# Kernel tuning notes

Hardware: AMD Instinct MI355X
Metric: run time of the kernel (lower is better)

The kernel has to match this reference:

```python
import jax, jax.numpy as jnp
import numpy as np

N = 50000   # nodes
E = 800000  # edges (avg degree 16)
D = 96      # feature dim (in = hidden = out)


def setup_inputs() -> dict:
    key = jax.random.key(0)
    ks = jax.random.split(key, 6)
    scale = 1.0 / np.sqrt(D)
    return {
        "x": jax.random.normal(ks[0], (N, D), jnp.float32),
        "edge_index": jax.random.randint(ks[1], (2, E), 0, N, dtype=jnp.int64),
        "W1": jax.random.normal(ks[2], (D, D), jnp.float32) * scale,
        "b1": jnp.zeros((D,), jnp.float32),
        "a1": jnp.full((1,), 0.25, jnp.float32),  # PReLU weight
        "W2": jax.random.normal(ks[3], (D, D), jnp.float32) * scale,
        "b2": jnp.zeros((D,), jnp.float32),
    }


def _gcn_conv(x, W, b, src, dst, norm, n):
    # GCNConv: linear transform, then degree-normalized scatter-add aggregation
    h = x @ W                               # [N, D_out]
    msg = h[src] * norm[:, None]            # gather + scale, [E+N, D_out]
    out = jax.ops.segment_sum(msg, dst, num_segments=n)
    return out + b


def reference(x, edge_index, W1, b1, a1, W2, b2):
    n = x.shape[0]
    # add self loops (PyG gcn_norm default, fill_value=1.0)
    loop = jnp.arange(n, dtype=edge_index.dtype)
    src = jnp.concatenate([edge_index[0], loop])
    dst = jnp.concatenate([edge_index[1], loop])
    # symmetric normalization: D^{-1/2} A D^{-1/2}
    ones = jnp.ones(src.shape[0], dtype=x.dtype)
    deg = jax.ops.segment_sum(ones, dst, num_segments=n)
    dinv = jnp.where(deg > 0, jax.lax.rsqrt(deg), 0.0)
    norm = dinv[src] * dinv[dst]

    h = _gcn_conv(x, W1, b1, src, dst, norm, n)
    h = jnp.where(h > 0, h, a1 * h)  # PReLU (dropout p=0.0 is a no-op)
    h = _gcn_conv(h, W2, b2, src, dst, norm, n)
    return h
```

## Files before the change

### kernel.cpp

```cpp
#include <hip/hip_runtime.h>
#include <hip/hip_bf16.h>

#define NNODES 50000
#define NEDGES 800000
#define DIM    96
#define NBUCK  196
#define PCHUNK 3125
#define TM     64
#define XPAD   104

typedef __attribute__((ext_vector_type(8))) short   short8;
typedef __attribute__((ext_vector_type(4))) float   float4v;

__device__ __forceinline__ float loadF(const void* p, long i, int isbf) {
    return isbf ? __bfloat162float(((const __hip_bfloat16*)p)[i])
                : ((const float*)p)[i];
}
__device__ __forceinline__ int clampN(int v) {
    return v < 0 ? 0 : (v >= NNODES ? NNODES - 1 : v);
}
__device__ __forceinline__ int edgeDst(const int* w, int e, int is64) {
    return clampN(is64 ? w[2 * (NEDGES + e)] : w[NEDGES + e]);
}
__device__ __forceinline__ int edgeSrc(const int* w, int e, int is64) {
    return clampN(is64 ? w[2 * e] : w[e]);
}

__global__ void k_sniff(const unsigned* __restrict__ xw,
                        const unsigned* __restrict__ ew,
                        int* __restrict__ flags,
                        int* __restrict__ bcnt,
                        int* __restrict__ bcur) {
    int lane = threadIdx.x;
    for (int i = lane; i < NBUCK; i += 64) { bcnt[i] = 0; bcur[i] = 0; }
    int bad = 0, nz = 0;
    for (int r = 0; r < 4; ++r) {
        unsigned w  = xw[lane + 64 * r];
        unsigned lo = w & 0xffffu;
        unsigned ex = (lo >> 7) & 0xffu;
        if (!(lo == 0u || (ex >= 90u && ex <= 145u))) bad++;
        unsigned o = ew[2 * (lane + 64 * r) + 1];
        if (o != 0u) nz++;
    }
    for (int off = 32; off; off >>= 1) {
        bad += __shfl_down(bad, off);
        nz  += __shfl_down(nz,  off);
    }
    if (lane == 0) {
        flags[0] = (bad <= 32) ? 1 : 0;
        flags[1] = (nz  <  4) ? 1 : 0;
    }
}

__global__ __launch_bounds__(256) void k_bcount(const int* __restrict__ w,
                                                int* __restrict__ bcnt,
                                                const int* __restrict__ flags) {
    __shared__ int h[NBUCK];
    const int is64 = flags[1];
    for (int i = threadIdx.x; i < NBUCK; i += 256) h[i] = 0;
    __syncthreads();
    const int nth = gridDim.x * blockDim.x;
    for (int e = blockIdx.x * blockDim.x + threadIdx.x; e < NEDGES; e += nth)
        atomicAdd(&h[edgeDst(w, e, is64) >> 8], 1);
    __syncthreads();
    for (int i = threadIdx.x; i < NBUCK; i += 256)
        if (h[i]) atomicAdd(&bcnt[i], h[i]);
}

__global__ __launch_bounds__(256) void k_part(const int* __restrict__ w,
                                              const int* __restrict__ bcnt,
                                              int* __restrict__ bcur,
                                              unsigned* __restrict__ ebuf,
                                              const int* __restrict__ flags) {
    __shared__ int sbase[256];
    __shared__ int h[NBUCK];
    __shared__ int base[NBUCK];
    const int is64 = flags[1];
    const int tid  = threadIdx.x;
    const int e0 = blockIdx.x * PCHUNK;
    const int e1 = (e0 + PCHUNK < NEDGES) ? e0 + PCHUNK : NEDGES;

    int v = (tid < NBUCK) ? bcnt[tid] : 0;
    sbase[tid] = v;
    __syncthreads();
    for (int off = 1; off < 256; off <<= 1) {
        int t = (tid >= off) ? sbase[tid - off] : 0;
        __syncthreads();
        sbase[tid] += t;
        __syncthreads();
    }
    int excl = sbase[tid] - v;
    __syncthreads();
    sbase[tid] = excl;
    if (tid < NBUCK) h[tid] = 0;
    __syncthreads();

    for (int e = e0 + tid; e < e1; e += 256)
        atomicAdd(&h[edgeDst(w, e, is64) >> 8], 1);
    __syncthreads();
    for (int i = tid; i < NBUCK; i += 256) {
        int c = h[i];
        base[i] = c ? sbase[i] + atomicAdd(&bcur[i], c) : 0;
        h[i] = 0;
    }
    __syncthreads();
    for (int e = e0 + tid; e < e1; e += 256) {
        int s = edgeSrc(w, e, is64);
        int d = edgeDst(w, e, is64);
        int b = d >> 8;
        int pos = base[b] + atomicAdd(&h[b], 1);
        ebuf[pos] = ((unsigned)d << 16) | (unsigned)s;
    }
}

__global__ __launch_bounds__(512) void k_csr(const unsigned* __restrict__ ebuf,
                                             const int* __restrict__ bcnt,
                                             int* __restrict__ rowptr,
                                             unsigned short* __restrict__ col,
                                             float* __restrict__ dinv) {
    __shared__ int gbase[256];
    __shared__ int h[256];
    __shared__ int sc[256];
    __shared__ int cur[256];
    const int b   = blockIdx.x;
    const int tid = threadIdx.x;

    if (tid < 256) gbase[tid] = (tid < NBUCK) ? bcnt[tid] : 0;
    __syncthreads();
    for (int off = 1; off < 256; off <<= 1) {
        int t = 0;
        if (tid < 256 && tid >= off) t = gbase[tid - off];
        __syncthreads();
        if (tid < 256) gbase[tid] += t;
        __syncthreads();
    }
    const int e0 = (b == 0) ? 0 : gbase[b - 1];
    const int e1 = gbase[b];
    __syncthreads();

    if (tid < 256) h[tid] = 0;
    __syncthreads();
    for (int e = e0 + tid; e < e1; e += 512)
        atomicAdd(&h[(ebuf[e] >> 16) & 255], 1);
    __syncthreads();
    int v = 0;
    if (tid < 256) { v = h[tid]; sc[tid] = v; }
    __syncthreads();
    for (int off = 1; off < 256; off <<= 1) {
        int t = 0;
        if (tid < 256 && tid >= off) t = sc[tid - off];
        __syncthreads();
        if (tid < 256) sc[tid] += t;
        __syncthreads();
    }
    if (tid < 256) {
        int start = e0 + sc[tid] - v;
        cur[tid] = start;
        int node = b * 256 + tid;
        if (node < NNODES) {
            rowptr[node] = start;
            dinv[node] = rsqrtf((float)v + 1.0f);
        }
    }
    if (b == 0 && tid == 0) rowptr[NNODES] = NEDGES;
    __syncthreads();
    for (int e = e0 + tid; e < e1; e += 512) {
        unsigned r = ebuf[e];
        int dl = (r >> 16) & 255;
        int pos = atomicAdd(&cur[dl], 1);
        col[pos] = (unsigned short)(r & 0xffffu);
    }
}

__global__ __launch_bounds__(256) void k_gemm_mfma(
        const void* __restrict__ X, int x_force_bf16,
        const void* __restrict__ W,
        const float* __restrict__ dinv,
        __hip_bfloat16* __restrict__ g,
        const int* __restrict__ flags) {
    __shared__ __hip_bfloat16 Xs[TM * XPAD];
    __shared__ __hip_bfloat16 Wt[DIM * XPAD];

    const int t    = threadIdx.x;
    const int fbf  = flags[0];
    const int xbf  = x_force_bf16 ? 1 : fbf;
    const int row0 = blockIdx.x * TM;

    for (int idx = t; idx < DIM * DIM; idx += 256) {
        int k = idx / DIM, n = idx - k * DIM;
        Wt[n * XPAD + k] = __float2bfloat16(loadF(W, idx, fbf));
    }
    for (int idx = t; idx < TM * DIM; idx += 256) {
        int r = idx / DIM, c = idx - r * DIM;
        int gr = row0 + r;
        float v = (gr < NNODES) ? loadF(X, (long)gr * DIM + c, xbf) : 0.f;
        Xs[r * XPAD + c] = __float2bfloat16(v);
    }
    __syncthreads();

    const int wave = t >> 6;
    const int lane = t & 63;
    const int m    = lane & 15;
    const int quad = lane >> 4;

    const short* xsp = (const short*)Xs;
    short8 a[3];
#pragma unroll
    for (int kt = 0; kt < 3; ++kt)
        a[kt] = *(const short8*)(xsp + (wave * 16 + m) * XPAD + kt * 32 + quad * 8);

    float dv[4];
#pragma unroll
    for (int r2 = 0; r2 < 4; ++r2) {
        int gr = row0 + wave * 16 + quad * 4 + r2;
        dv[r2] = (gr < NNODES) ? dinv[gr] : 0.f;
    }

    const short* wtp = (const short*)Wt;
#pragma unroll
    for (int nt = 0; nt < 6; ++nt) {
        float4v acc = {0.f, 0.f, 0.f, 0.f};
#pragma unroll
        for (int kt = 0; kt < 3; ++kt) {
            short8 b = *(const short8*)(wtp + (nt * 16 + m) * XPAD + kt * 32 + quad * 8);
            acc = __builtin_amdgcn_mfma_f32_16x16x32_bf16(a[kt], b, acc, 0, 0, 0);
        }
#pragma unroll
        for (int r2 = 0; r2 < 4; ++r2) {
            int gr = row0 + wave * 16 + quad * 4 + r2;
            if (gr < NNODES)
                g[(size_t)gr * DIM + nt * 16 + m] = __float2bfloat16(acc[r2] * dv[r2]);
        }
    }
}

__global__ __launch_bounds__(256) void k_aggr(
        const __hip_bfloat16* __restrict__ g,
        const int* __restrict__ rowptr,
        const unsigned short* __restrict__ col,
        const float* __restrict__ dinv,
        const void* __restrict__ b,
        const void* __restrict__ a1,
        void* __restrict__ out,
        const int* __restrict__ flags, int prelu) {
    const int wave = threadIdx.x >> 6;
    const int lane = threadIdx.x & 63;
    const int row  = blockIdx.x * 4 + wave;
    if (row >= NNODES) return;
    const int fbf = flags[0];
    const __hip_bfloat162* gv = (const __hip_bfloat162*)g;
    const int c = lane;

    float2 acc = {0.f, 0.f};
    if (c < 48) acc = __bfloat1622float2(gv[(size_t)row * 48 + c]);

    const int p0 = rowptr[row], p1 = rowptr[row + 1];
    int i = p0;
    for (; i + 16 <= p1; i += 16) {
        int s[16];
#pragma unroll
        for (int k = 0; k < 16; ++k) s[k] = col[i + k];
        if (c < 48) {
            float2 v[16];
#pragma unroll
            for (int k = 0; k < 16; ++k)
                v[k] = __bfloat1622float2(gv[(size_t)s[k] * 48 + c]);
            float2 t0, t1, t2, t3;
            t0.x = (v[0].x + v[1].x) + (v[2].x + v[3].x);
            t0.y = (v[0].y + v[1].y) + (v[2].y + v[3].y);
            t1.x = (v[4].x + v[5].x) + (v[6].x + v[7].x);
            t1.y = (v[4].y + v[5].y) + (v[6].y + v[7].y);
            t2.x = (v[8].x + v[9].x) + (v[10].x + v[11].x);
            t2.y = (v[8].y + v[9].y) + (v[10].y + v[11].y);
            t3.x = (v[12].x + v[13].x) + (v[14].x + v[15].x);
            t3.y = (v[12].y + v[13].y) + (v[14].y + v[15].y);
            acc.x += (t0.x + t1.x) + (t2.x + t3.x);
            acc.y += (t0.y + t1.y) + (t2.y + t3.y);
        }
    }
    for (; i + 8 <= p1; i += 8) {
        int s[8];
#pragma unroll
        for (int k = 0; k < 8; ++k) s[k] = col[i + k];
        if (c < 48) {
            float2 v[8];
#pragma unroll
            for (int k = 0; k < 8; ++k)
                v[k] = __bfloat1622float2(gv[(size_t)s[k] * 48 + c]);
            acc.x += ((v[0].x + v[1].x) + (v[2].x + v[3].x))
                   + ((v[4].x + v[5].x) + (v[6].x + v[7].x));
            acc.y += ((v[0].y + v[1].y) + (v[2].y + v[3].y))
                   + ((v[4].y + v[5].y) + (v[6].y + v[7].y));
        }
    }
    for (; i + 4 <= p1; i += 4) {
        int s0 = col[i], s1 = col[i+1], s2 = col[i+2], s3 = col[i+3];
        if (c < 48) {
            float2 v0 = __bfloat1622float2(gv[(size_t)s0 * 48 + c]);
            float2 v1 = __bfloat1622float2(gv[(size_t)s1 * 48 + c]);
            float2 v2 = __bfloat1622float2(gv[(size_t)s2 * 48 + c]);
            float2 v3 = __bfloat1622float2(gv[(size_t)s3 * 48 + c]);
            acc.x += (v0.x + v1.x) + (v2.x + v3.x);
            acc.y += (v0.y + v1.y) + (v2.y + v3.y);
        }
    }
    for (; i < p1; ++i) {
        int s = col[i];
        if (c < 48) {
            float2 v = __bfloat1622float2(gv[(size_t)s * 48 + c]);
            acc.x += v.x; acc.y += v.y;
        }
    }

    if (c < 48) {
        float dv = dinv[row];
        float vx = dv * acc.x + loadF(b, 2 * c,     fbf);
        float vy = dv * acc.y + loadF(b, 2 * c + 1, fbf);
        if (prelu) {
            float alpha = loadF(a1, 0, fbf);
            vx = vx > 0.f ? vx : alpha * vx;
            vy = vy > 0.f ? vy : alpha * vy;
            ((__hip_bfloat162*)out)[(size_t)row * 48 + c] =
                __halves2bfloat162(__float2bfloat16(vx), __float2bfloat16(vy));
        } else if (fbf) {
            ((__hip_bfloat162*)out)[(size_t)row * 48 + c] =
                __halves2bfloat162(__float2bfloat16(vx), __float2bfloat16(vy));
        } else {
            float2 o; o.x = vx; o.y = vy;
            ((float2*)out)[(size_t)row * 48 + c] = o;
        }
    }
}

extern "C" void kernel_launch(void* const* d_in, const int* in_sizes, int n_in,
                              void* d_out, int out_size, void* d_ws, size_t ws_size,
                              hipStream_t stream) {
    const void* x  = d_in[0];
    const int*  ei = (const int*)d_in[1];
    const void* W1 = d_in[2];
    const void* b1 = d_in[3];
    const void* a1 = d_in[4];
    const void* W2 = d_in[5];
    const void* b2 = d_in[6];

    size_t off = 0;
    auto alloc = [&](size_t bytes) { size_t p = off; off = (off + bytes + 255) & ~(size_t)255; return p; };
    char* ws = (char*)d_ws;
    int*            flags  = (int*)           (ws + alloc(1024));
    float*          dinv   = (float*)         (ws + alloc((size_t)NNODES * 4));
    int*            bcnt   = (int*)           (ws + alloc((size_t)NBUCK * 4));
    int*            bcur   = (int*)           (ws + alloc((size_t)NBUCK * 4));
    int*            rowptr = (int*)           (ws + alloc(((size_t)NNODES + 1) * 4));
    unsigned*       ebuf   = (unsigned*)      (ws + alloc((size_t)NEDGES * 4));
    unsigned short* col    = (unsigned short*)(ws + alloc((size_t)NEDGES * 2));
    __hip_bfloat16* g      = (__hip_bfloat16*)(ws + alloc((size_t)NNODES * DIM * 2));
    __hip_bfloat16* g2     = (__hip_bfloat16*)(ws + alloc((size_t)NNODES * DIM * 2));
    if (ws_size < off) return;

    k_sniff<<<1, 64, 0, stream>>>((const unsigned*)x, (const unsigned*)ei, flags, bcnt, bcur);

    k_bcount<<<256, 256, 0, stream>>>(ei, bcnt, flags);
    k_part  <<<(NEDGES + PCHUNK - 1) / PCHUNK, 256, 0, stream>>>(ei, bcnt, bcur, ebuf, flags);
    k_csr   <<<NBUCK, 512, 0, stream>>>(ebuf, bcnt, rowptr, col, dinv);

    const int gemm_grid = (NNODES + TM - 1) / TM;
    const int aggr_grid = (NNODES + 3) / 4;

    k_gemm_mfma<<<gemm_grid, 256, 0, stream>>>(x, 0, W1, dinv, g, flags);
    k_aggr<<<aggr_grid, 256, 0, stream>>>(g, rowptr, col, dinv, b1, a1, g2, flags, 1);

    k_gemm_mfma<<<gemm_grid, 256, 0, stream>>>(g2, 1, W2, dinv, g, flags);
    k_aggr<<<aggr_grid, 256, 0, stream>>>(g, rowptr, col, dinv, b2, a1, d_out, flags, 0);
}
```

Before: 235.5 us.

## Fuse CSR build into one grid-barrier kernel and fuse layer-1 aggregation with GEMM2

Merges the sniff, bucket-count, partition and CSR kernels into a single persistent kernel that synchronises its 256 blocks through a software global barrier on a device atomic counter. Edges are packed in LDS and per-block histograms replace global atomics. The first aggregation is fused with the second GEMM, so PReLU output stays in LDS instead of round-tripping through global memory. GEMM input staging also switches to float4 loads. This removes several launches and one intermediate buffer, but relies on all 256 blocks being co-resident for the spin barrier, and the fused aggregation+GEMM uses fewer, larger blocks.

```diff
diff --git a/kernel.cpp b/kernel.cpp
--- a/kernel.cpp
+++ b/kernel.cpp
@@ -5,12 +5,17 @@
 #define NEDGES 800000
 #define DIM    96
 #define NBUCK  196
-#define PCHUNK 3125
 #define TM     64
 #define XPAD   104
+#define PBLK   256
+#define PTHR   512
+#define PCH    3125
+#define HPAD   256
 
 typedef __attribute__((ext_vector_type(8))) short   short8;
 typedef __attribute__((ext_vector_type(4))) float   float4v;
+
+__device__ int g_bar[2] = {0, 0};
 
 __device__ __forceinline__ float loadF(const void* p, long i, int isbf) {
     return isbf ? __bfloat162float(((const __hip_bfloat16*)p)[i])
@@ -26,154 +31,163 @@
     return clampN(is64 ? w[2 * e] : w[e]);
 }
 
-__global__ void k_sniff(const unsigned* __restrict__ xw,
-                        const unsigned* __restrict__ ew,
-                        int* __restrict__ flags,
-                        int* __restrict__ bcnt,
-                        int* __restrict__ bcur) {
-    int lane = threadIdx.x;
-    for (int i = lane; i < NBUCK; i += 64) { bcnt[i] = 0; bcur[i] = 0; }
-    int bad = 0, nz = 0;
-    for (int r = 0; r < 4; ++r) {
-        unsigned w  = xw[lane + 64 * r];
+__device__ __forceinline__ void gbar(int slot) {
+    __syncthreads();
+    if (threadIdx.x == 0) {
+        __threadfence();
+        atomicAdd(&g_bar[slot], 1);
+        while (atomicAdd(&g_bar[slot], 0) < PBLK) __builtin_amdgcn_s_sleep(2);
+        __threadfence();
+    }
+    __syncthreads();
+}
+
+__global__ __launch_bounds__(512) void k_prep(
+        const unsigned* __restrict__ xw,
+        const int* __restrict__ ew,
+        int* __restrict__ flags,
+        int* __restrict__ hist,
+        unsigned* __restrict__ ebuf,
+        int* __restrict__ rowptr,
+        unsigned short* __restrict__ col,
+        float* __restrict__ dinv) {
+    __shared__ unsigned pack[PCH];
+    __shared__ int h[NBUCK];
+    __shared__ int sb[256];
+    __shared__ int tot[256];
+    __shared__ int base[NBUCK];
+    __shared__ int h256[256];
+    __shared__ int sc[256];
+    __shared__ int cur[256];
+    __shared__ int sniff[2];
+
+    const int tid = threadIdx.x;
+    const int blk = blockIdx.x;
+
+    if (tid < 2) sniff[tid] = 0;
+    __syncthreads();
+    if (tid < 256) {
+        unsigned w  = xw[tid];
         unsigned lo = w & 0xffffu;
         unsigned ex = (lo >> 7) & 0xffu;
-        if (!(lo == 0u || (ex >= 90u && ex <= 145u))) bad++;
-        unsigned o = ew[2 * (lane + 64 * r) + 1];
-        if (o != 0u) nz++;
-    }
-    for (int off = 32; off; off >>= 1) {
-        bad += __shfl_down(bad, off);
-        nz  += __shfl_down(nz,  off);
-    }
-    if (lane == 0) {
-        flags[0] = (bad <= 32) ? 1 : 0;
-        flags[1] = (nz  <  4) ? 1 : 0;
-    }
-}
-
-__global__ __launch_bounds__(256) void k_bcount(const int* __restrict__ w,
-                                                int* __restrict__ bcnt,
-                                                const int* __restrict__ flags) {
-    __shared__ int h[NBUCK];
-    const int is64 = flags[1];
-    for (int i = threadIdx.x; i < NBUCK; i += 256) h[i] = 0;
-    __syncthreads();
-    const int nth = gridDim.x * blockDim.x;
-    for (int e = blockIdx.x * blockDim.x + threadIdx.x; e < NEDGES; e += nth)
-        atomicAdd(&h[edgeDst(w, e, is64) >> 8], 1);
-    __syncthreads();
-    for (int i = threadIdx.x; i < NBUCK; i += 256)
-        if (h[i]) atomicAdd(&bcnt[i], h[i]);
-}
-
-__global__ __launch_bounds__(256) void k_part(const int* __restrict__ w,
-                                              const int* __restrict__ bcnt,
-                                              int* __restrict__ bcur,
-                                              unsigned* __restrict__ ebuf,
-                                              const int* __restrict__ flags) {
-    __shared__ int sbase[256];
-    __shared__ int h[NBUCK];
-    __shared__ int base[NBUCK];
-    const int is64 = flags[1];
-    const int tid  = threadIdx.x;
-    const int e0 = blockIdx.x * PCHUNK;
-    const int e1 = (e0 + PCHUNK < NEDGES) ? e0 + PCHUNK : NEDGES;
-
-    int v = (tid < NBUCK) ? bcnt[tid] : 0;
-    sbase[tid] = v;
+        if (!(lo == 0u || (ex >= 90u && ex <= 145u))) atomicAdd(&sniff[0], 1);
+        if (((const unsigned*)ew)[2 * tid + 1] != 0u)  atomicAdd(&sniff[1], 1);
+    }
+    __syncthreads();
+    const int fbf  = (sniff[0] <= 32) ? 1 : 0;
+    const int is64 = (sniff[1] <  4) ? 1 : 0;
+    if (blk == 0 && tid == 0) { flags[0] = fbf; flags[1] = is64; }
+
+    for (int i = tid; i < NBUCK; i += PTHR) h[i] = 0;
+    __syncthreads();
+    const int e0 = blk * PCH;
+    for (int k = tid; k < PCH; k += PTHR) {
+        int e = e0 + k;
+        int s = edgeSrc(ew, e, is64);
+        int d = edgeDst(ew, e, is64);
+        pack[k] = ((unsigned)d << 16) | (unsigned)s;
+        atomicAdd(&h[d >> 8], 1);
+    }
+    __syncthreads();
+    for (int i = tid; i < NBUCK; i += PTHR) hist[blk * HPAD + i] = h[i];
+
+    gbar(0);
+
+    if (tid < 256) tot[tid] = 0;
+    int pre = 0;
+    if (tid < NBUCK) {
+        int t = 0, p = 0;
+        for (int j = 0; j < PBLK; ++j) {
+            int v = hist[j * HPAD + tid];
+            t += v;
+            if (j < blk) p += v;
+        }
+        tot[tid] = t;
+        pre = p;
+    }
+    __syncthreads();
+    if (tid < 256) sb[tid] = tot[tid];
     __syncthreads();
     for (int off = 1; off < 256; off <<= 1) {
-        int t = (tid >= off) ? sbase[tid - off] : 0;
+        int t2 = 0;
+        if (tid < 256 && tid >= off) t2 = sb[tid - off];
         __syncthreads();
-        sbase[tid] += t;
+        if (tid < 256) sb[tid] += t2;
         __syncthreads();
     }
-    int excl = sbase[tid] - v;
-    __syncthreads();
-    sbase[tid] = excl;
-    if (tid < NBUCK) h[tid] = 0;
-    __syncthreads();
-
-    for (int e = e0 + tid; e < e1; e += 256)
-        atomicAdd(&h[edgeDst(w, e, is64) >> 8], 1);
-    __syncthreads();
-    for (int i = tid; i < NBUCK; i += 256) {
-        int c = h[i];
-        base[i] = c ? sbase[i] + atomicAdd(&bcur[i], c) : 0;
-        h[i] = 0;
-    }
-    __syncthreads();
-    for (int e = e0 + tid; e < e1; e += 256) {
-        int s = edgeSrc(w, e, is64);
-        int d = edgeDst(w, e, is64);
-        int b = d >> 8;
+    if (tid < NBUCK) {
+        base[tid] = (sb[tid] - tot[tid]) + pre;
+        h[tid] = 0;
+    }
+    __syncthreads();
+    for (int k = tid; k < PCH; k += PTHR) {
+        unsigned r = pack[k];
+        int b = r >> 24;
         int pos = base[b] + atomicAdd(&h[b], 1);
-        ebuf[pos] = ((unsigned)d << 16) | (unsigned)s;
-    }
-}
-
-__global__ __launch_bounds__(512) void k_csr(const unsigned* __restrict__ ebuf,
-                                             const int* __restrict__ bcnt,
-                                             int* __restrict__ rowptr,
-                                             unsigned short* __restrict__ col,
-                                             float* __restrict__ dinv) {
-    __shared__ int gbase[256];
-    __shared__ int h[256];
-    __shared__ int sc[256];
-    __shared__ int cur[256];
-    const int b   = blockIdx.x;
-    const int tid = threadIdx.x;
-
-    if (tid < 256) gbase[tid] = (tid < NBUCK) ? bcnt[tid] : 0;
+        ebuf[pos] = r;
+    }
+
+    gbar(1);
+
+    if (blk >= NBUCK) return;
+    const int be0 = sb[blk] - tot[blk];
+    const int be1 = sb[blk];
+    if (tid < 256) h256[tid] = 0;
+    __syncthreads();
+    for (int e = be0 + tid; e < be1; e += PTHR)
+        atomicAdd(&h256[(ebuf[e] >> 16) & 255], 1);
+    __syncthreads();
+    int v = 0;
+    if (tid < 256) { v = h256[tid]; sc[tid] = v; }
     __syncthreads();
     for (int off = 1; off < 256; off <<= 1) {
-        int t = 0;
-        if (tid < 256 && tid >= off) t = gbase[tid - off];
+        int t2 = 0;
+        if (tid < 256 && tid >= off) t2 = sc[tid - off];
         __syncthreads();
-        if (tid < 256) gbase[tid] += t;
+        if (tid < 256) sc[tid] += t2;
         __syncthreads();
     }
-    const int e0 = (b == 0) ? 0 : gbase[b - 1];
-    const int e1 = gbase[b];
-    __syncthreads();
-
-    if (tid < 256) h[tid] = 0;
-    __syncthreads();
-    for (int e = e0 + tid; e < e1; e += 512)
-        atomicAdd(&h[(ebuf[e] >> 16) & 255], 1);
-    __syncthreads();
-    int v = 0;
-    if (tid < 256) { v = h[tid]; sc[tid] = v; }
-    __syncthreads();
-    for (int off = 1; off < 256; off <<= 1) {
-        int t = 0;
-        if (tid < 256 && tid >= off) t = sc[tid - off];
-        __syncthreads();
-        if (tid < 256) sc[tid] += t;
-        __syncthreads();
-    }
     if (tid < 256) {
-        int start = e0 + sc[tid] - v;
+        int start = be0 + sc[tid] - v;
         cur[tid] = start;
-        int node = b * 256 + tid;
+        int node = blk * 256 + tid;
         if (node < NNODES) {
             rowptr[node] = start;
             dinv[node] = rsqrtf((float)v + 1.0f);
         }
     }
-    if (b == 0 && tid == 0) rowptr[NNODES] = NEDGES;
-    __syncthreads();
-    for (int e = e0 + tid; e < e1; e += 512) {
+    if (blk == 0 && tid == 0) rowptr[NNODES] = NEDGES;
+    __syncthreads();
+    for (int e = be0 + tid; e < be1; e += PTHR) {
         unsigned r = ebuf[e];
-        int dl = (r >> 16) & 255;
-        int pos = atomicAdd(&cur[dl], 1);
+        int pos = atomicAdd(&cur[(r >> 16) & 255], 1);
         col[pos] = (unsigned short)(r & 0xffffu);
     }
 }
 
+__device__ __forceinline__ void stage_wt(const void* W, int fbf,
+                                         __hip_bfloat16* Wt, int t) {
+    if (!fbf) {
+        const float4* Wv = (const float4*)W;
+        for (int idx = t; idx < DIM * DIM / 4; idx += 256) {
+            int k = idx / (DIM / 4);
+            int n = (idx - k * (DIM / 4)) * 4;
+            float4 w4 = Wv[idx];
+            Wt[(n + 0) * XPAD + k] = __float2bfloat16(w4.x);
+            Wt[(n + 1) * XPAD + k] = __float2bfloat16(w4.y);
+            Wt[(n + 2) * XPAD + k] = __float2bfloat16(w4.z);
+            Wt[(n + 3) * XPAD + k] = __float2bfloat16(w4.w);
+        }
+    } else {
+        for (int idx = t; idx < DIM * DIM; idx += 256) {
+            int k = idx / DIM, n = idx - k * DIM;
+            Wt[n * XPAD + k] = __float2bfloat16(loadF(W, idx, 1));
+        }
+    }
+}
+
 __global__ __launch_bounds__(256) void k_gemm_mfma(
-        const void* __restrict__ X, int x_force_bf16,
+        const void* __restrict__ X,
         const void* __restrict__ W,
         const float* __restrict__ dinv,
         __hip_bfloat16* __restrict__ g,
@@ -181,20 +195,35 @@
     __shared__ __hip_bfloat16 Xs[TM * XPAD];
     __shared__ __hip_bfloat16 Wt[DIM * XPAD];
 
-    const int t    = threadIdx.x;
+    const int t = threadIdx.x;
+    if (blockIdx.x == 0 && t == 0) {
+        atomicExch(&g_bar[0], 0);
+        atomicExch(&g_bar[1], 0);
+    }
     const int fbf  = flags[0];
-    const int xbf  = x_force_bf16 ? 1 : fbf;
     const int row0 = blockIdx.x * TM;
 
-    for (int idx = t; idx < DIM * DIM; idx += 256) {
-        int k = idx / DIM, n = idx - k * DIM;
-        Wt[n * XPAD + k] = __float2bfloat16(loadF(W, idx, fbf));
-    }
-    for (int idx = t; idx < TM * DIM; idx += 256) {
-        int r = idx / DIM, c = idx - r * DIM;
-        int gr = row0 + r;
-        float v = (gr < NNODES) ? loadF(X, (long)gr * DIM + c, xbf) : 0.f;
-        Xs[r * XPAD + c] = __float2bfloat16(v);
+    stage_wt(W, fbf, Wt, t);
+    if (!fbf) {
+        const float4* Xv = (const float4*)X;
+        for (int idx = t; idx < TM * DIM / 4; idx += 256) {
+            int r = idx / (DIM / 4);
+            int c = (idx - r * (DIM / 4)) * 4;
+            int gr = row0 + r;
+            float4 vv = {0.f, 0.f, 0.f, 0.f};
+            if (gr < NNODES) vv = Xv[(size_t)gr * (DIM / 4) + (c >> 2)];
+            *(__hip_bfloat162*)&Xs[r * XPAD + c] =
+                __halves2bfloat162(__float2bfloat16(vv.x), __float2bfloat16(vv.y));
+            *(__hip_bfloat162*)&Xs[r * XPAD + c + 2] =
+                __halves2bfloat162(__float2bfloat16(vv.z), __float2bfloat16(vv.w));
+        }
+    } else {
+        for (int idx = t; idx < TM * DIM; idx += 256) {
+            int r = idx / DIM, c = idx - r * DIM;
+            int gr = row0 + r;
+            float vv = (gr < NNODES) ? loadF(X, (long)gr * DIM + c, 1) : 0.f;
+            Xs[r * XPAD + c] = __float2bfloat16(vv);
+        }
     }
     __syncthreads();
 
@@ -230,6 +259,152 @@
             int gr = row0 + wave * 16 + quad * 4 + r2;
             if (gr < NNODES)
                 g[(size_t)gr * DIM + nt * 16 + m] = __float2bfloat16(acc[r2] * dv[r2]);
+        }
+    }
+}
+
+__device__ __forceinline__ float2 gather_row(
+        const __hip_bfloat162* __restrict__ gv,
+        const int* __restrict__ rowptr,
+        const unsigned short* __restrict__ col,
+        int row, int c) {
+    float2 acc = {0.f, 0.f};
+    if (c < 48) acc = __bfloat1622float2(gv[(size_t)row * 48 + c]);
+    const int p0 = rowptr[row], p1 = rowptr[row + 1];
+    int i = p0;
+    for (; i + 16 <= p1; i += 16) {
+        int s[16];
+#pragma unroll
+        for (int k = 0; k < 16; ++k) s[k] = col[i + k];
+        if (c < 48) {
+            float2 v[16];
+#pragma unroll
+            for (int k = 0; k < 16; ++k)
+                v[k] = __bfloat1622float2(gv[(size_t)s[k] * 48 + c]);
+            float2 t0, t1, t2, t3;
+            t0.x = (v[0].x + v[1].x) + (v[2].x + v[3].x);
+            t0.y = (v[0].y + v[1].y) + (v[2].y + v[3].y);
+            t1.x = (v[4].x + v[5].x) + (v[6].x + v[7].x);
+            t1.y = (v[4].y + v[5].y) + (v[6].y + v[7].y);
+            t2.x = (v[8].x + v[9].x) + (v[10].x + v[11].x);
+            t2.y = (v[8].y + v[9].y) + (v[10].y + v[11].y);
+            t3.x = (v[12].x + v[13].x) + (v[14].x + v[15].x);
+            t3.y = (v[12].y + v[13].y) + (v[14].y + v[15].y);
+            acc.x += (t0.x + t1.x) + (t2.x + t3.x);
+            acc.y += (t0.y + t1.y) + (t2.y + t3.y);
+        }
+    }
+    for (; i + 8 <= p1; i += 8) {
+        int s[8];
+#pragma unroll
+        for (int k = 0; k < 8; ++k) s[k] = col[i + k];
+        if (c < 48) {
+            float2 v[8];
+#pragma unroll
+            for (int k = 0; k < 8; ++k)
+                v[k] = __bfloat1622float2(gv[(size_t)s[k] * 48 + c]);
+            acc.x += ((v[0].x + v[1].x) + (v[2].x + v[3].x))
+                   + ((v[4].x + v[5].x) + (v[6].x + v[7].x));
+            acc.y += ((v[0].y + v[1].y) + (v[2].y + v[3].y))
+                   + ((v[4].y + v[5].y) + (v[6].y + v[7].y));
+        }
+    }
+    for (; i + 4 <= p1; i += 4) {
+        int s0 = col[i], s1 = col[i + 1], s2 = col[i + 2], s3 = col[i + 3];
+        if (c < 48) {
+            float2 v0 = __bfloat1622float2(gv[(size_t)s0 * 48 + c]);
+            float2 v1 = __bfloat1622float2(gv[(size_t)s1 * 48 + c]);
+            float2 v2 = __bfloat1622float2(gv[(size_t)s2 * 48 + c]);
+            float2 v3 = __bfloat1622float2(gv[(size_t)s3 * 48 + c]);
+            acc.x += (v0.x + v1.x) + (v2.x + v3.x);
+            acc.y += (v0.y + v1.y) + (v2.y + v3.y);
+        }
+    }
+    for (; i < p1; ++i) {
+        int s = col[i];
+        if (c < 48) {
+            float2 v = __bfloat1622float2(gv[(size_t)s * 48 + c]);
+            acc.x += v.x; acc.y += v.y;
+        }
+    }
+    return acc;
+}
+
+__global__ __launch_bounds__(256) void k_aggr_gemm(
+        const __hip_bfloat16* __restrict__ g,
+        const int* __restrict__ rowptr,
+        const unsigned short* __restrict__ col,
+        const float* __restrict__ dinv,
+        const void* __restrict__ b1,
+        const void* __restrict__ a1,
+        const void* __restrict__ W2,
+        __hip_bfloat16* __restrict__ g2,
+        const int* __restrict__ flags) {
+    __shared__ __hip_bfloat16 Hs[TM * XPAD];
+    __shared__ __hip_bfloat16 Wt[DIM * XPAD];
+
+    const int t = threadIdx.x;
+    const int fbf  = flags[0];
+    const int row0 = blockIdx.x * TM;
+    const int wave = t >> 6;
+    const int lane = t & 63;
+    const int c = lane;
+
+    stage_wt(W2, fbf, Wt, t);
+
+    const __hip_bfloat162* gv = (const __hip_bfloat162*)g;
+    const float alpha = loadF(a1, 0, fbf);
+    float bx = 0.f, by = 0.f;
+    if (c < 48) { bx = loadF(b1, 2 * c, fbf); by = loadF(b1, 2 * c + 1, fbf); }
+
+#pragma unroll 1
+    for (int p = 0; p < TM / 4; ++p) {
+        const int r   = p * 4 + wave;
+        const int row = row0 + r;
+        float vx = 0.f, vy = 0.f;
+        if (row < NNODES) {
+            float2 acc = gather_row(gv, rowptr, col, row, c);
+            float dv = dinv[row];
+            vx = dv * acc.x + bx;
+            vy = dv * acc.y + by;
+            vx = vx > 0.f ? vx : alpha * vx;
+            vy = vy > 0.f ? vy : alpha * vy;
+        }
+        if (c < 48)
+            *(__hip_bfloat162*)&Hs[r * XPAD + 2 * c] =
+                __halves2bfloat162(__float2bfloat16(vx), __float2bfloat16(vy));
+    }
+    __syncthreads();
+
+    const int m    = lane & 15;
+    const int quad = lane >> 4;
+    const short* xsp = (const short*)Hs;
+    short8 afr[3];
+#pragma unroll
+    for (int kt = 0; kt < 3; ++kt)
+        afr[kt] = *(const short8*)(xsp + (wave * 16 + m) * XPAD + kt * 32 + quad * 8);
+
+    float dvv[4];
+#pragma unroll
+    for (int r2 = 0; r2 < 4; ++r2) {
+        int gr = row0 + wave * 16 + quad * 4 + r2;
+        dvv[r2] = (gr < NNODES) ? dinv[gr] : 0.f;
+    }
+
+    const short* wtp = (const short*)Wt;
+#pragma unroll
+    for (int nt = 0; nt < 6; ++nt) {
+        float4v acc4 = {0.f, 0.f, 0.f, 0.f};
+#pragma unroll
+        for (int kt = 0; kt < 3; ++kt) {
+            short8 bfr = *(const short8*)(wtp + (nt * 16 + m) * XPAD + kt * 32 + quad * 8);
+            acc4 = __builtin_amdgcn_mfma_f32_16x16x32_bf16(afr[kt], bfr, acc4, 0, 0, 0);
+        }
+#pragma unroll
+        for (int r2 = 0; r2 < 4; ++r2) {
+            int gr = row0 + wave * 16 + quad * 4 + r2;
+            if (gr < NNODES)
+                g2[(size_t)gr * DIM + nt * 16 + m] = __float2bfloat16(acc4[r2] * dvv[r2]);
         }
     }
 }
@@ -248,69 +423,9 @@
     const int row  = blockIdx.x * 4 + wave;
     if (row >= NNODES) return;
     const int fbf = flags[0];
-    const __hip_bfloat162* gv = (const __hip_bfloat162*)g;
     const int c = lane;
 
-    float2 acc = {0.f, 0.f};
-    if (c < 48) acc = __bfloat1622float2(gv[(size_t)row * 48 + c]);
-
-    const int p0 = rowptr[row], p1 = rowptr[row + 1];
-    int i = p0;
-    for (; i + 16 <= p1; i += 16) {
-        int s[16];
-#pragma unroll
-        for (int k = 0; k < 16; ++k) s[k] = col[i + k];
-        if (c < 48) {
-            float2 v[16];
-#pragma unroll
-            for (int k = 0; k < 16; ++k)
-                v[k] = __bfloat1622float2(gv[(size_t)s[k] * 48 + c]);
-            float2 t0, t1, t2, t3;
-            t0.x = (v[0].x + v[1].x) + (v[2].x + v[3].x);
-            t0.y = (v[0].y + v[1].y) + (v[2].y + v[3].y);
-            t1.x = (v[4].x + v[5].x) + (v[6].x + v[7].x);
-            t1.y = (v[4].y + v[5].y) + (v[6].y + v[7].y);
-            t2.x = (v[8].x + v[9].x) + (v[10].x + v[11].x);
-            t2.y = (v[8].y + v[9].y) + (v[10].y + v[11].y);
-            t3.x = (v[12].x + v[13].x) + (v[14].x + v[15].x);
-            t3.y = (v[12].y + v[13].y) + (v[14].y + v[15].y);
-            acc.x += (t0.x + t1.x) + (t2.x + t3.x);
-            acc.y += (t0.y + t1.y) + (t2.y + t3.y);
-        }
-    }
-    for (; i + 8 <= p1; i += 8) {
-        int s[8];
-#pragma unroll
-        for (int k = 0; k < 8; ++k) s[k] = col[i + k];
-        if (c < 48) {
-            float2 v[8];
-#pragma unroll
-            for (int k = 0; k < 8; ++k)
-                v[k] = __bfloat1622float2(gv[(size_t)s[k] * 48 + c]);
-            acc.x += ((v[0].x + v[1].x) + (v[2].x + v[3].x))
-                   + ((v[4].x + v[5].x) + (v[6].x + v[7].x));
-            acc.y += ((v[0].y + v[1].y) + (v[2].y + v[3].y))
-                   + ((v[4].y + v[5].y) + (v[6].y + v[7].y));
-        }
-    }
-    for (; i + 4 <= p1; i += 4) {
-        int s0 = col[i], s1 = col[i+1], s2 = col[i+2], s3 = col[i+3];
-        if (c < 48) {
-            float2 v0 = __bfloat1622float2(gv[(size_t)s0 * 48 + c]);
-            float2 v1 = __bfloat1622float2(gv[(size_t)s1 * 48 + c]);
-            float2 v2 = __bfloat1622float2(gv[(size_t)s2 * 48 + c]);
-            float2 v3 = __bfloat1622float2(gv[(size_t)s3 * 48 + c]);
-            acc.x += (v0.x + v1.x) + (v2.x + v3.x);
-            acc.y += (v0.y + v1.y) + (v2.y + v3.y);
-        }
-    }
-    for (; i < p1; ++i) {
-        int s = col[i];
-        if (c < 48) {
-            float2 v = __bfloat1622float2(gv[(size_t)s * 48 + c]);
-            acc.x += v.x; acc.y += v.y;
-        }
-    }
+    float2 acc = gather_row((const __hip_bfloat162*)g, rowptr, col, row, c);
 
     if (c < 48) {
         float dv = dinv[row];
@@ -348,27 +463,21 @@
     char* ws = (char*)d_ws;
     int*            flags  = (int*)           (ws + alloc(1024));
     float*          dinv   = (float*)         (ws + alloc((size_t)NNODES * 4));
-    int*            bcnt   = (int*)           (ws + alloc((size_t)NBUCK * 4));
-    int*            bcur   = (int*)           (ws + alloc((size_t)NBUCK * 4));
     int*            rowptr = (int*)           (ws + alloc(((size_t)NNODES + 1) * 4));
+    int*            hist   = (int*)           (ws + alloc((size_t)PBLK * HPAD * 4));
     unsigned*       ebuf   = (unsigned*)      (ws + alloc((size_t)NEDGES * 4));
     unsigned short* col    = (unsigned short*)(ws + alloc((size_t)NEDGES * 2));
     __hip_bfloat16* g      = (__hip_bfloat16*)(ws + alloc((size_t)NNODES * DIM * 2));
     __hip_bfloat16* g2     = (__hip_bfloat16*)(ws + alloc((size_t)NNODES * DIM * 2));
     if (ws_size < off) return;
 
-    k_sniff<<<1, 64, 0, stream>>>((const unsigned*)x, (const unsigned*)ei, flags, bcnt, bcur);
-
-    k_bcount<<<256, 256, 0, stream>>>(ei, bcnt, flags);
-    k_part  <<<(NEDGES + PCHUNK - 1) / PCHUNK, 256, 0, stream>>>(ei, bcnt, bcur, ebuf, flags);
-    k_csr   <<<NBUCK, 512, 0, stream>>>(ebuf, bcnt, rowptr, col, dinv);
+    k_prep<<<PBLK, PTHR, 0, stream>>>((const unsigned*)x, ei, flags, hist,
+                                      ebuf, rowptr, col, dinv);
 
     const int gemm_grid = (NNODES + TM - 1) / TM;
     const int aggr_grid = (NNODES + 3) / 4;
 
-    k_gemm_mfma<<<gemm_grid, 256, 0, stream>>>(x, 0, W1, dinv, g, flags);
-    k_aggr<<<aggr_grid, 256, 0, stream>>>(g, rowptr, col, dinv, b1, a1, g2, flags, 1);
-
-    k_gemm_mfma<<<gemm_grid, 256, 0, stream>>>(g2, 1, W2, dinv, g, flags);
-    k_aggr<<<aggr_grid, 256, 0, stream>>>(g, rowptr, col, dinv, b2, a1, d_out, flags, 0);
-}
+    k_gemm_mfma<<<gemm_grid, 256, 0, stream>>>(x, W1, dinv, g, flags);
+    k_aggr_gemm<<<gemm_grid, 256, 0, stream>>>(g, rowptr, col, dinv, b1, a1, W2, g2, flags);
+    k_aggr<<<aggr_grid, 256, 0, stream>>>(g2, rowptr, col, dinv, b2, a1, d_out, flags, 0);
+}
```

Result: slower. 267.3 us (+13.5%).
